# Performance work log

Measured on AMD Instinct MI355X. Metric: run time of the kernel, lower is better.

Reference implementation:

```python
import jax, jax.numpy as jnp
import numpy as np


def setup_inputs() -> dict:
    key = jax.random.key(0)
    ks = jax.random.split(key, 7)
    T, D, V = 2048, 1024, 28  # frames, encoder hidden, vocab_size
    s = 0.05  # keras 'random_normal' initializer stddev
    return {
        "x": jax.random.normal(ks[0], (1, T, D), jnp.float32),
        "Wa": jax.random.normal(ks[1], (1, V), jnp.float32) * s,
        "Ua": jax.random.normal(ks[2], (1, D), jnp.float32) * s,
        "Va": jax.random.normal(ks[3], (1, 1), jnp.float32) * s,
        "Wo": jax.random.normal(ks[4], (V, V), jnp.float32) * s,
        "Uo": jax.random.normal(ks[5], (V, D), jnp.float32) * s,
        "Co": jax.random.normal(ks[6], (V, D), jnp.float32) * s,
    }


def reference(x, Wa, Ua, Va, Wo, Uo, Co):
    # Source uses only the first batch element: x = x[0]
    xb = x[0]                      # (T, D)
    V = Wo.shape[0]
    D = Uo.shape[1]
    # Ua . x[j] is constant across outer steps t (source recomputes it; math identical)
    ux = xb @ Ua[0]                # (T,)

    def step(carry, xt):
        Y, H = carry               # Y: (V,) previous output, H: (D,) previous frame
        prev = Wa[0] @ Y           # scalar: Wa . Yanterior
        scores = Va[0, 0] * jnp.tanh(ux + prev)   # (T,)
        # Source applies K.softmax (axis=-1) to scores of shape (T,1,1):
        # softmax over a size-1 axis -> all ones. Reproduced faithfully.
        w = jax.nn.softmax(scores[:, None], axis=-1)   # (T, 1), all ones
        context = (xb * w).sum(axis=0)                 # (D,)
        y = jax.nn.sigmoid(Wo @ Y + Uo @ H + Co @ context)  # (V,)
        return (y, xt), y          # Hanterior <- x[t]

    init = (jnp.zeros((V,), xb.dtype), jnp.zeros((D,), xb.dtype))
    _, ys = jax.lax.scan(step, init, xb)   # ys: (T, V)
    return ys[None]                        # (1, T, V)
```

## Files before the change

kernel.cpp:

```cpp
#include <hip/hip_runtime.h>

#define T_FRAMES 2048
#define D_DIM    1024
#define V_DIM    28
#define BSTRIDE  32
#define LOG2E_F  1.44269504088896f

#define CHUNK    16
#define WARM     24
#define NCHUNK   (T_FRAMES / CHUNK)

#define RPB      4
#define NB_PREP  (T_FRAMES / RPB)

__global__ __launch_bounds__(256) void prep_kernel(const float* __restrict__ x,
                                                   const float* __restrict__ Uo,
                                                   const float* __restrict__ Co,
                                                   float* __restrict__ cpart,
                                                   float* __restrict__ Bmat) {
    int tid = threadIdx.x, b = blockIdx.x;
    __shared__ float xs[RPB * D_DIM];
    __shared__ float cs[D_DIM];

    const float4* xb4 = (const float4*)(x + (size_t)b * RPB * D_DIM);
    float4 csum = make_float4(0.f, 0.f, 0.f, 0.f);
#pragma unroll
    for (int r = 0; r < RPB; ++r) {
        float4 v = xb4[r * (D_DIM / 4) + tid];
        ((float4*)xs)[r * (D_DIM / 4) + tid] = v;
        csum.x += v.x; csum.y += v.y; csum.z += v.z; csum.w += v.w;
    }
    ((float4*)cs)[tid] = csum;
    __syncthreads();

    int wave = tid >> 6, lane = tid & 63;

    float4 u[7][4];
#pragma unroll
    for (int q = 0; q < 7; ++q) {
        const float4* u4 = (const float4*)(Uo + (size_t)(wave * 7 + q) * D_DIM);
#pragma unroll
        for (int m = 0; m < 4; ++m) u[q][m] = u4[lane + 64 * m];
    }

#pragma unroll
    for (int q = 0; q < 7; ++q) {
        int i = wave * 7 + q;
        const float4* c4 = (const float4*)(Co + (size_t)i * D_DIM);
        float acc = 0.f;
#pragma unroll
        for (int m = 0; m < 4; ++m) {
            float4 a = c4[lane + 64 * m];
            float4 d = ((const float4*)cs)[lane + 64 * m];
            acc += a.x * d.x + a.y * d.y + a.z * d.z + a.w * d.w;
        }
#pragma unroll
        for (int off = 32; off > 0; off >>= 1) acc += __shfl_down(acc, off);
        if (lane == 0) cpart[(size_t)i * NB_PREP + b] = acc;
    }

#pragma unroll
    for (int r = 0; r < RPB; ++r) {
        int t = b * RPB + r + 1;
        if (t >= T_FRAMES) break;
        float4 xv[4];
#pragma unroll
        for (int m = 0; m < 4; ++m)
            xv[m] = ((const float4*)xs)[r * (D_DIM / 4) + lane + 64 * m];
#pragma unroll
        for (int q = 0; q < 7; ++q) {
            float acc = 0.f;
#pragma unroll
            for (int m = 0; m < 4; ++m) {
                acc = fmaf(u[q][m].x, xv[m].x, acc);
                acc = fmaf(u[q][m].y, xv[m].y, acc);
                acc = fmaf(u[q][m].z, xv[m].z, acc);
                acc = fmaf(u[q][m].w, xv[m].w, acc);
            }
#pragma unroll
            for (int off = 32; off > 0; off >>= 1) acc += __shfl_down(acc, off);
            if (lane == 0) Bmat[(size_t)t * BSTRIDE + wave * 7 + q] = acc * LOG2E_F;
        }
    }

    if (b == 0 && tid < BSTRIDE) Bmat[tid] = 0.f;
}

#define RL(j) __int_as_float(__builtin_amdgcn_readlane(yi_, j))

#define DECL_W(j) float w##j = act ? Wo[(size_t)lane * V_DIM + j] * LOG2E_F : 0.f;
#define REP28(X) X(0) X(1) X(2) X(3) X(4) X(5) X(6) X(7) X(8) X(9) X(10) X(11) \
                 X(12) X(13) X(14) X(15) X(16) X(17) X(18) X(19) X(20) X(21)  \
                 X(22) X(23) X(24) X(25) X(26) X(27)

#define STEP(bval, ydst)                                                     \
    {                                                                        \
        int yi_ = __float_as_int(y);                                         \
        float a0 = (bval) + cik, a1 = 0.f, a2 = 0.f, a3 = 0.f;               \
        a0 = fmaf(w0,  RL(0),  a0);  a1 = fmaf(w1,  RL(1),  a1);             \
        a2 = fmaf(w2,  RL(2),  a2);  a3 = fmaf(w3,  RL(3),  a3);             \
        a0 = fmaf(w4,  RL(4),  a0);  a1 = fmaf(w5,  RL(5),  a1);             \
        a2 = fmaf(w6,  RL(6),  a2);  a3 = fmaf(w7,  RL(7),  a3);             \
        a0 = fmaf(w8,  RL(8),  a0);  a1 = fmaf(w9,  RL(9),  a1);             \
        a2 = fmaf(w10, RL(10), a2);  a3 = fmaf(w11, RL(11), a3);             \
        a0 = fmaf(w12, RL(12), a0);  a1 = fmaf(w13, RL(13), a1);             \
        a2 = fmaf(w14, RL(14), a2);  a3 = fmaf(w15, RL(15), a3);             \
        a0 = fmaf(w16, RL(16), a0);  a1 = fmaf(w17, RL(17), a1);             \
        a2 = fmaf(w18, RL(18), a2);  a3 = fmaf(w19, RL(19), a3);             \
        a0 = fmaf(w20, RL(20), a0);  a1 = fmaf(w21, RL(21), a1);             \
        a2 = fmaf(w22, RL(22), a2);  a3 = fmaf(w23, RL(23), a3);             \
        a0 = fmaf(w24, RL(24), a0);  a1 = fmaf(w25, RL(25), a1);             \
        a2 = fmaf(w26, RL(26), a2);  a3 = fmaf(w27, RL(27), a3);             \
        float acc_ = (a0 + a1) + (a2 + a3);                                  \
        y = __builtin_amdgcn_rcpf(1.f + __builtin_amdgcn_exp2f(-acc_));      \
        ydst = y;                                                            \
    }

#define SSTEP(n)                                                             \
    {                                                                        \
        int tn_ = (t + 1 < T_FRAMES) ? t + 1 : 0;                            \
        float bn_ = Bmat[(size_t)tn_ * BSTRIDE + bl];          \
        STEP(bcur, yb##n)                                                    \
        bcur = bn_; ++t;                                                     \
    }

__global__ __launch_bounds__(64, 1) void scan_kernel(const float* __restrict__ Bmat,
                                                     const float* __restrict__ cpart,
                                                     const float* __restrict__ Wo,
                                                     float* __restrict__ out) {
    int lane = threadIdx.x;
    bool act = lane < V_DIM;
    int bl   = lane & (BSTRIDE - 1);

    REP28(DECL_W)

    const float4* cp4 = (const float4*)(cpart + (size_t)(act ? lane : 0) * NB_PREP);
    float cs0 = 0.f, cs1 = 0.f, cs2 = 0.f, cs3 = 0.f;
#pragma unroll
    for (int m = 0; m < NB_PREP / 4; m += 4) {
        float4 a = cp4[m],     e = cp4[m + 1];
        float4 f = cp4[m + 2], g = cp4[m + 3];
        cs0 += (a.x + a.y) + (a.z + a.w);
        cs1 += (e.x + e.y) + (e.z + e.w);
        cs2 += (f.x + f.y) + (f.z + f.w);
        cs3 += (g.x + g.y) + (g.z + g.w);
    }
    float cik = act ? ((cs0 + cs1) + (cs2 + cs3)) * LOG2E_F : 0.f;

    int tstore = blockIdx.x * CHUNK;
    int t0     = tstore - WARM; if (t0 < 0) t0 = 0;
    int nwarm  = tstore - t0;

    float y    = 0.f;
    int   t    = t0;
    float bcur = Bmat[(size_t)t0 * BSTRIDE + bl];

    for (int s = 0; s < nwarm; ++s) {
        float bnext = Bmat[(size_t)(t + 1) * BSTRIDE + bl];
        float dump;
        STEP(bcur, dump)
        (void)dump;
        bcur = bnext; ++t;
    }

    float yb0, yb1, yb2, yb3, yb4, yb5, yb6, yb7;
    float yb8, yb9, yb10, yb11, yb12, yb13, yb14, yb15;
    SSTEP(0)  SSTEP(1)  SSTEP(2)  SSTEP(3)
    SSTEP(4)  SSTEP(5)  SSTEP(6)  SSTEP(7)
    SSTEP(8)  SSTEP(9)  SSTEP(10) SSTEP(11)
    SSTEP(12) SSTEP(13) SSTEP(14) SSTEP(15)

    if (act) {
        float* op = out + (size_t)tstore * V_DIM + lane;
        op[0  * V_DIM] = yb0;  op[1  * V_DIM] = yb1;
        op[2  * V_DIM] = yb2;  op[3  * V_DIM] = yb3;
        op[4  * V_DIM] = yb4;  op[5  * V_DIM] = yb5;
        op[6  * V_DIM] = yb6;  op[7  * V_DIM] = yb7;
        op[8  * V_DIM] = yb8;  op[9  * V_DIM] = yb9;
        op[10 * V_DIM] = yb10; op[11 * V_DIM] = yb11;
        op[12 * V_DIM] = yb12; op[13 * V_DIM] = yb13;
        op[14 * V_DIM] = yb14; op[15 * V_DIM] = yb15;
    }
}

extern "C" void kernel_launch(void* const* d_in, const int* in_sizes, int n_in,
                              void* d_out, int out_size, void* d_ws, size_t ws_size,
                              hipStream_t stream) {
    const float* x  = (const float*)d_in[0];
    const float* Wo = (const float*)d_in[4];
    const float* Uo = (const float*)d_in[5];
    const float* Co = (const float*)d_in[6];
    float* out = (float*)d_out;

    float* W     = (float*)d_ws;
    float* cpart = W;
    float* Bmat  = W + 16384;

    prep_kernel<<<NB_PREP, 256, 0, stream>>>(x, Uo, Co, cpart, Bmat);
    scan_kernel<<<NCHUNK,  64,  0, stream>>>(Bmat, cpart, Wo, out);
}
```

Measured before the change: 97.88 us.

## Halve scan chunk size, transpose cpart layout, and parallelize context reduction

The scan chunk shrinks from 16 to 8 steps, so twice as many blocks each run a shorter serial dependency chain, while the warmup length per block stays the same. The cpart partials are stored block-major with a stride of 32, and the scan kernel reduces them cooperatively across all 64 lanes with double accumulators and xor shuffles. Previously each lane serially summed 512 values. Wo rows are loaded as float4 vectors, and the prep kernel issues the Uo loads before its LDS stores to overlap memory latency. The tradeoff is more redundant warmup compute in total and a shared-memory sync in the scan kernel.

```diff
diff --git a/kernel.cpp b/kernel.cpp
--- a/kernel.cpp
+++ b/kernel.cpp
@@ -4,9 +4,10 @@
 #define D_DIM    1024
 #define V_DIM    28
 #define BSTRIDE  32
+#define CSTRIDE  32
 #define LOG2E_F  1.44269504088896f
 
-#define CHUNK    16
+#define CHUNK    8
 #define WARM     24
 #define NCHUNK   (T_FRAMES / CHUNK)
 
@@ -22,26 +23,33 @@
     __shared__ float xs[RPB * D_DIM];
     __shared__ float cs[D_DIM];
 
+    int wave = tid >> 6, lane = tid & 63;
+
     const float4* xb4 = (const float4*)(x + (size_t)b * RPB * D_DIM);
-    float4 csum = make_float4(0.f, 0.f, 0.f, 0.f);
-#pragma unroll
-    for (int r = 0; r < RPB; ++r) {
-        float4 v = xb4[r * (D_DIM / 4) + tid];
-        ((float4*)xs)[r * (D_DIM / 4) + tid] = v;
-        csum.x += v.x; csum.y += v.y; csum.z += v.z; csum.w += v.w;
-    }
+    float4 xv0 = xb4[0 * (D_DIM / 4) + tid];
+    float4 xv1 = xb4[1 * (D_DIM / 4) + tid];
+    float4 xv2 = xb4[2 * (D_DIM / 4) + tid];
+    float4 xv3 = xb4[3 * (D_DIM / 4) + tid];
+
+    float4 u[7][4];
+#pragma unroll
+    for (int q = 0; q < 7; ++q) {
+        const float4* u4 = (const float4*)(Uo + (size_t)(wave * 7 + q) * D_DIM);
+#pragma unroll
+        for (int m = 0; m < 4; ++m) u[q][m] = u4[lane + 64 * m];
+    }
+
+    ((float4*)xs)[0 * (D_DIM / 4) + tid] = xv0;
+    ((float4*)xs)[1 * (D_DIM / 4) + tid] = xv1;
+    ((float4*)xs)[2 * (D_DIM / 4) + tid] = xv2;
+    ((float4*)xs)[3 * (D_DIM / 4) + tid] = xv3;
+    float4 csum;
+    csum.x = (xv0.x + xv1.x) + (xv2.x + xv3.x);
+    csum.y = (xv0.y + xv1.y) + (xv2.y + xv3.y);
+    csum.z = (xv0.z + xv1.z) + (xv2.z + xv3.z);
+    csum.w = (xv0.w + xv1.w) + (xv2.w + xv3.w);
     ((float4*)cs)[tid] = csum;
     __syncthreads();
-
-    int wave = tid >> 6, lane = tid & 63;
-
-    float4 u[7][4];
-#pragma unroll
-    for (int q = 0; q < 7; ++q) {
-        const float4* u4 = (const float4*)(Uo + (size_t)(wave * 7 + q) * D_DIM);
-#pragma unroll
-        for (int m = 0; m < 4; ++m) u[q][m] = u4[lane + 64 * m];
-    }
 
 #pragma unroll
     for (int q = 0; q < 7; ++q) {
@@ -56,8 +64,10 @@
         }
 #pragma unroll
         for (int off = 32; off > 0; off >>= 1) acc += __shfl_down(acc, off);
-        if (lane == 0) cpart[(size_t)i * NB_PREP + b] = acc;
-    }
+        if (lane == 0) cpart[(size_t)b * CSTRIDE + i] = acc;
+    }
+    if (tid == 0)
+        *(float4*)(cpart + (size_t)b * CSTRIDE + V_DIM) = make_float4(0.f, 0.f, 0.f, 0.f);
 
 #pragma unroll
     for (int r = 0; r < RPB; ++r) {
@@ -87,11 +97,6 @@
 }
 
 #define RL(j) __int_as_float(__builtin_amdgcn_readlane(yi_, j))
-
-#define DECL_W(j) float w##j = act ? Wo[(size_t)lane * V_DIM + j] * LOG2E_F : 0.f;
-#define REP28(X) X(0) X(1) X(2) X(3) X(4) X(5) X(6) X(7) X(8) X(9) X(10) X(11) \
-                 X(12) X(13) X(14) X(15) X(16) X(17) X(18) X(19) X(20) X(21)  \
-                 X(22) X(23) X(24) X(25) X(26) X(27)
 
 #define STEP(bval, ydst)                                                     \
     {                                                                        \
@@ -131,21 +136,44 @@
     int lane = threadIdx.x;
     bool act = lane < V_DIM;
     int bl   = lane & (BSTRIDE - 1);
-
-    REP28(DECL_W)
-
-    const float4* cp4 = (const float4*)(cpart + (size_t)(act ? lane : 0) * NB_PREP);
-    float cs0 = 0.f, cs1 = 0.f, cs2 = 0.f, cs3 = 0.f;
-#pragma unroll
-    for (int m = 0; m < NB_PREP / 4; m += 4) {
-        float4 a = cp4[m],     e = cp4[m + 1];
-        float4 f = cp4[m + 2], g = cp4[m + 3];
-        cs0 += (a.x + a.y) + (a.z + a.w);
-        cs1 += (e.x + e.y) + (e.z + e.w);
-        cs2 += (f.x + f.y) + (f.z + f.w);
-        cs3 += (g.x + g.y) + (g.z + g.w);
-    }
-    float cik = act ? ((cs0 + cs1) + (cs2 + cs3)) * LOG2E_F : 0.f;
+    __shared__ float cfin[32];
+
+    const float4* wrow = (const float4*)(Wo + (size_t)(act ? lane : 0) * V_DIM);
+    float4 wqa = wrow[0], wqb = wrow[1], wqc = wrow[2], wqd = wrow[3];
+    float4 wqe = wrow[4], wqf = wrow[5], wqg = wrow[6];
+
+    int q8 = lane & 7;
+    int bo = lane >> 3;
+    const float4* cp4 = (const float4*)cpart;
+    double d0 = 0.0, d1 = 0.0, d2 = 0.0, d3 = 0.0;
+#pragma unroll
+    for (int m = 0; m < NB_PREP / 8; ++m) {
+        float4 v = cp4[(size_t)(m * 8 + bo) * (CSTRIDE / 4) + q8];
+        d0 += v.x; d1 += v.y; d2 += v.z; d3 += v.w;
+    }
+#pragma unroll
+    for (int off = 8; off < 64; off <<= 1) {
+        d0 += __shfl_xor(d0, off);
+        d1 += __shfl_xor(d1, off);
+        d2 += __shfl_xor(d2, off);
+        d3 += __shfl_xor(d3, off);
+    }
+    if (bo == 0) {
+        cfin[q8 * 4 + 0] = (float)d0;
+        cfin[q8 * 4 + 1] = (float)d1;
+        cfin[q8 * 4 + 2] = (float)d2;
+        cfin[q8 * 4 + 3] = (float)d3;
+    }
+    __syncthreads();
+    float cik = cfin[lane & 31] * LOG2E_F;
+
+    float w0  = wqa.x * LOG2E_F, w1  = wqa.y * LOG2E_F, w2  = wqa.z * LOG2E_F, w3  = wqa.w * LOG2E_F;
+    float w4  = wqb.x * LOG2E_F, w5  = wqb.y * LOG2E_F, w6  = wqb.z * LOG2E_F, w7  = wqb.w * LOG2E_F;
+    float w8  = wqc.x * LOG2E_F, w9  = wqc.y * LOG2E_F, w10 = wqc.z * LOG2E_F, w11 = wqc.w * LOG2E_F;
+    float w12 = wqd.x * LOG2E_F, w13 = wqd.y * LOG2E_F, w14 = wqd.z * LOG2E_F, w15 = wqd.w * LOG2E_F;
+    float w16 = wqe.x * LOG2E_F, w17 = wqe.y * LOG2E_F, w18 = wqe.z * LOG2E_F, w19 = wqe.w * LOG2E_F;
+    float w20 = wqf.x * LOG2E_F, w21 = wqf.y * LOG2E_F, w22 = wqf.z * LOG2E_F, w23 = wqf.w * LOG2E_F;
+    float w24 = wqg.x * LOG2E_F, w25 = wqg.y * LOG2E_F, w26 = wqg.z * LOG2E_F, w27 = wqg.w * LOG2E_F;
 
     int tstore = blockIdx.x * CHUNK;
     int t0     = tstore - WARM; if (t0 < 0) t0 = 0;
@@ -164,22 +192,15 @@
     }
 
     float yb0, yb1, yb2, yb3, yb4, yb5, yb6, yb7;
-    float yb8, yb9, yb10, yb11, yb12, yb13, yb14, yb15;
-    SSTEP(0)  SSTEP(1)  SSTEP(2)  SSTEP(3)
-    SSTEP(4)  SSTEP(5)  SSTEP(6)  SSTEP(7)
-    SSTEP(8)  SSTEP(9)  SSTEP(10) SSTEP(11)
-    SSTEP(12) SSTEP(13) SSTEP(14) SSTEP(15)
+    SSTEP(0) SSTEP(1) SSTEP(2) SSTEP(3)
+    SSTEP(4) SSTEP(5) SSTEP(6) SSTEP(7)
 
     if (act) {
         float* op = out + (size_t)tstore * V_DIM + lane;
-        op[0  * V_DIM] = yb0;  op[1  * V_DIM] = yb1;
-        op[2  * V_DIM] = yb2;  op[3  * V_DIM] = yb3;
-        op[4  * V_DIM] = yb4;  op[5  * V_DIM] = yb5;
-        op[6  * V_DIM] = yb6;  op[7  * V_DIM] = yb7;
-        op[8  * V_DIM] = yb8;  op[9  * V_DIM] = yb9;
-        op[10 * V_DIM] = yb10; op[11 * V_DIM] = yb11;
-        op[12 * V_DIM] = yb12; op[13 * V_DIM] = yb13;
-        op[14 * V_DIM] = yb14; op[15 * V_DIM] = yb15;
+        op[0 * V_DIM] = yb0; op[1 * V_DIM] = yb1;
+        op[2 * V_DIM] = yb2; op[3 * V_DIM] = yb3;
+        op[4 * V_DIM] = yb4; op[5 * V_DIM] = yb5;
+        op[6 * V_DIM] = yb6; op[7 * V_DIM] = yb7;
     }
 }
 
@@ -194,7 +215,7 @@
 
     float* W     = (float*)d_ws;
     float* cpart = W;
-    float* Bmat  = W + 16384;
+    float* Bmat  = W + NB_PREP * CSTRIDE;
 
     prep_kernel<<<NB_PREP, 256, 0, stream>>>(x, Uo, Co, cpart, Bmat);
     scan_kernel<<<NCHUNK,  64,  0, stream>>>(Bmat, cpart, Wo, out);
```

Result: faster. 94.64 us (-3.3%).
